# Optimization experiments

Hardware: AMD Instinct MI355X
Metric: run time of the kernel (lower is better)

## Reference

```python
import jax, jax.numpy as jnp
import numpy as np

N = 100000      # nodes
E = 1600000     # edges (avg degree 16)
D_IN, HID, D_OUT = 128, 64, 64


def setup_inputs() -> dict:
    key = jax.random.key(0)
    ks = jax.random.split(key, 32)
    rn = lambda k, shape, s=0.1: jax.random.normal(k, shape, jnp.float32) * s
    inp = {
        "x": jax.random.normal(ks[0], (N, D_IN), jnp.float32),
        "edge_index": jax.random.randint(ks[1], (2, E), 0, N, dtype=jnp.int32),
        # GAT layer 1: in=128, heads=2, C=64, concat -> 128
        "w1": rn(ks[2], (D_IN, 2 * HID)), "as1": rn(ks[3], (2, HID)),
        "ad1": rn(ks[4], (2, HID)), "b1": rn(ks[5], (2 * HID,)),
        # GAT layer 2: in=128, heads=2, C=64, concat -> 128
        "w2": rn(ks[6], (2 * HID, 2 * HID)), "as2": rn(ks[7], (2, HID)),
        "ad2": rn(ks[8], (2, HID)), "b2": rn(ks[9], (2 * HID,)),
        # GAT layer 3: in=128, heads=1, C=64, mean -> 64
        "w3": rn(ks[10], (2 * HID, D_OUT)), "as3": rn(ks[11], (1, D_OUT)),
        "ad3": rn(ks[12], (1, D_OUT)), "b3": rn(ks[13], (D_OUT,)),
        # BatchNorm (eval mode: running stats)
        "g1": 1.0 + rn(ks[14], (2 * HID,)), "be1": rn(ks[15], (2 * HID,)),
        "m1": rn(ks[16], (2 * HID,), 0.01), "v1": 1.0 + 0.1 * jax.random.uniform(ks[17], (2 * HID,)),
        "g2": 1.0 + rn(ks[18], (2 * HID,)), "be2": rn(ks[19], (2 * HID,)),
        "m2": rn(ks[20], (2 * HID,), 0.01), "v2": 1.0 + 0.1 * jax.random.uniform(ks[21], (2 * HID,)),
        "g3": 1.0 + rn(ks[22], (D_OUT,)), "be3": rn(ks[23], (D_OUT,)),
        "m3": rn(ks[24], (D_OUT,), 0.01), "v3": 1.0 + 0.1 * jax.random.uniform(ks[25], (D_OUT,)),
    }
    return inp


def _gat(h, W, a_s, a_d, b, src, dst, n, heads, concat):
    """PyG GATConv (eval, add_self_loops already applied to src/dst)."""
    C = a_s.shape[1]
    xl = (h @ W).reshape(n, heads, C)                      # [N,H,C]
    es = jnp.sum(xl * a_s, axis=-1)                        # [N,H] att_src . x
    ed = jnp.sum(xl * a_d, axis=-1)                        # [N,H]
    e = jax.nn.leaky_relu(es[src] + ed[dst], 0.2)          # [E',H]
    mx = jax.ops.segment_max(e, dst, num_segments=n)       # segment softmax over dst
    ex = jnp.exp(e - mx[dst])
    den = jax.ops.segment_sum(ex, dst, num_segments=n)
    alpha = ex / (den[dst] + 1e-16)                        # [E',H]
    out = jax.ops.segment_sum(xl[src] * alpha[:, :, None], dst, num_segments=n)
    out = out.reshape(n, heads * C) if concat else out.mean(axis=1)
    return out + b


def _bn(z, g, be, m, v):
    return (z - m) * jax.lax.rsqrt(v + 1e-5) * g + be


def reference(x, edge_index, w1, as1, ad1, b1, w2, as2, ad2, b2, w3, as3, ad3, b3,
              g1, be1, m1, v1, g2, be2, m2, v2, g3, be3, m3, v3):
    n = x.shape[0]
    loop = jnp.arange(n, dtype=edge_index.dtype)
    src = jnp.concatenate([edge_index[0], loop])           # GATConv add_self_loops=True
    dst = jnp.concatenate([edge_index[1], loop])
    z = jax.nn.relu(_bn(_gat(x, w1, as1, ad1, b1, src, dst, n, 2, True), g1, be1, m1, v1))
    z = jax.nn.relu(_bn(_gat(z, w2, as2, ad2, b2, src, dst, n, 2, True), g2, be2, m2, v2))
    z = _bn(_gat(z, w3, as3, ad3, b3, src, dst, n, 1, False), g3, be3, m3, v3)
    return z
```

## Files before the change

kernel.cpp:

```cpp
#include <hip/hip_runtime.h>
#include <hip/hip_bf16.h>
#include <cstdint>
#include <cstddef>

#define SCAN_CHUNK 2048
#define NBLK 512
#define BSH 8

typedef short bf16x8 __attribute__((ext_vector_type(8)));
typedef float f32x4 __attribute__((ext_vector_type(4)));

__device__ __forceinline__ float leaky02(float x) { return x > 0.f ? x : 0.2f * x; }
__device__ __forceinline__ float bflo(unsigned u) { return __uint_as_float(u << 16); }
__device__ __forceinline__ float bfhi(unsigned u) { return __uint_as_float(u & 0xFFFF0000u); }
__device__ __forceinline__ unsigned short f2bf(float f) {
  __hip_bfloat16 h = __float2bfloat16(f);
  return *(unsigned short*)&h;
}
__device__ __forceinline__ unsigned pack2bf(float a, float b) {
  return (unsigned)f2bf(a) | ((unsigned)f2bf(b) << 16);
}

__global__ void scan_pass1(const int* __restrict__ cnt, int* __restrict__ bsum, int n) {
  __shared__ int red[4];
  int b = blockIdx.x, t = threadIdx.x;
  int base = b * SCAN_CHUNK;
  int s = 0;
  for (int i = t; i < SCAN_CHUNK; i += 256) {
    int idx = base + i;
    if (idx < n) s += cnt[idx];
  }
  for (int off = 32; off; off >>= 1) s += __shfl_xor(s, off);
  int lane = t & 63, wid = t >> 6;
  if (lane == 0) red[wid] = s;
  __syncthreads();
  if (t == 0) bsum[b] = red[0] + red[1] + red[2] + red[3];
}

__global__ void scan_pass2(int* __restrict__ bsum, int nb, int* __restrict__ totp) {
  if (threadIdx.x == 0) {
    int run = 0;
    for (int i = 0; i < nb; ++i) { int v = bsum[i]; bsum[i] = run; run += v; }
    *totp = run;
  }
}

__global__ void scan_pass3(const int* __restrict__ cnt, const int* __restrict__ bsum,
                           int* __restrict__ out, int n) {
  __shared__ int wsum[4];
  int b = blockIdx.x, t = threadIdx.x;
  int idx0 = b * SCAN_CHUNK + t * 8;
  int vals[8];
  int s = 0;
#pragma unroll
  for (int i = 0; i < 8; ++i) {
    int id = idx0 + i;
    int v = (id < n) ? cnt[id] : 0;
    vals[i] = s; s += v;
  }
  int lane = t & 63, wid = t >> 6;
  int incl = s;
  for (int off = 1; off < 64; off <<= 1) {
    int o = __shfl_up(incl, off);
    if (lane >= off) incl += o;
  }
  if (lane == 63) wsum[wid] = incl;
  __syncthreads();
  if (t == 0) { int r = 0; for (int i = 0; i < 4; ++i) { int v = wsum[i]; wsum[i] = r; r += v; } }
  __syncthreads();
  int texcl = incl - s + wsum[wid] + bsum[b];
#pragma unroll
  for (int i = 0; i < 8; ++i) {
    int id = idx0 + i;
    if (id < n) out[id] = texcl + vals[i];
  }
}

__global__ void bucketA(const int* __restrict__ dst, int* __restrict__ H,
                        int E, int NB, int chunk) {
  __shared__ int hist[512];
  int b = blockIdx.x, t = threadIdx.x;
  hist[t] = 0; hist[t + 256] = 0;
  __syncthreads();
  int e0 = b * chunk, e1 = min(E, e0 + chunk);
  for (int e = e0 + t; e < e1; e += 256) atomicAdd(&hist[dst[e] >> BSH], 1);
  __syncthreads();
  for (int k = t; k < NB; k += 256) H[k * NBLK + b] = hist[k];
}

__global__ void bucketB(const int* __restrict__ src, const int* __restrict__ dst,
                        const int* __restrict__ O, unsigned* __restrict__ binned,
                        int E, int NB, int chunk) {
  __shared__ int cur[512];
  int b = blockIdx.x, t = threadIdx.x;
  for (int k = t; k < NB; k += 256) cur[k] = O[k * NBLK + b];
  __syncthreads();
  int e0 = b * chunk, e1 = min(E, e0 + chunk);
  for (int e = e0 + t; e < e1; e += 256) {
    int d = dst[e];
    int k = d >> BSH;
    int pos = atomicAdd(&cur[k], 1);
    binned[pos] = (unsigned)src[e] | ((unsigned)(d & 255) << 24);
  }
}

__global__ void bucketC(const unsigned* __restrict__ binned, const int* __restrict__ O,
                        int* __restrict__ rowp, int* __restrict__ col,
                        int N, int E, int NB) {
  __shared__ int cnt2[256];
  __shared__ int cur2[256];
  __shared__ int wsum[4];
  int k = blockIdx.x, t = threadIdx.x;
  int base = O[k * NBLK];
  int end  = (k + 1 < NB) ? O[(k + 1) * NBLK] : E;
  cnt2[t] = 0;
  __syncthreads();
  for (int e = base + t; e < end; e += 256) atomicAdd(&cnt2[binned[e] >> 24], 1);
  __syncthreads();
  int v = cnt2[t];
  int incl = v;
  int lane = t & 63, wid = t >> 6;
  for (int off = 1; off < 64; off <<= 1) {
    int o = __shfl_up(incl, off);
    if (lane >= off) incl += o;
  }
  if (lane == 63) wsum[wid] = incl;
  __syncthreads();
  if (t == 0) { int r = 0; for (int i = 0; i < 4; ++i) { int x = wsum[i]; wsum[i] = r; r += x; } }
  __syncthreads();
  int excl = incl - v + wsum[wid];
  int g = (k << BSH) + t;
  if (g <= N) rowp[g] = base + excl;
  cur2[t] = excl;
  __syncthreads();
  for (int e = base + t; e < end; e += 256) {
    unsigned p = binned[e];
    int pos = atomicAdd(&cur2[p >> 24], 1);
    col[base + pos] = (int)(p & 0xFFFFFFu);
  }
}

__global__ void convert_x(const float* __restrict__ x, unsigned* __restrict__ out, int n4) {
  int i = blockIdx.x * blockDim.x + threadIdx.x;
  if (i >= n4) return;
  float4 v = ((const float4*)x)[i];
  uint2 o;
  o.x = pack2bf(v.x, v.y);
  o.y = pack2bf(v.z, v.w);
  ((uint2*)out)[i] = o;
}

__global__ void prep_w(const float* __restrict__ w1, const float* __restrict__ w2,
                       const float* __restrict__ w3,
                       unsigned short* __restrict__ t1, unsigned short* __restrict__ t2,
                       unsigned short* __restrict__ t3) {
  int b = blockIdx.x, t = threadIdx.x;
  const float* W; unsigned short* T; int NO; int e;
  if (b < 64)      { W = w1; T = t1; NO = 128; e = b * 256 + t; }
  else if (b < 128){ W = w2; T = t2; NO = 128; e = (b - 64) * 256 + t; }
  else             { W = w3; T = t3; NO = 64;  e = (b - 128) * 256 + t; }
  int c = e >> 7, k = e & 127;
  T[c * 128 + k] = f2bf(W[k * NO + c]);
}

template<int NO>
__launch_bounds__(256)
__global__ void gemm_mfma(const unsigned short* __restrict__ Xb,
                          const unsigned short* __restrict__ Wt,
                          unsigned short* __restrict__ Y, int n,
                          const float* __restrict__ as, const float* __restrict__ ad,
                          float* __restrict__ es, float* __restrict__ ed) {
  constexpr int NT = NO / 16;
  const int wid = threadIdx.x >> 6, lane = threadIdx.x & 63;
  const int wr0 = (blockIdx.x * 4 + wid) * 32;
  if (wr0 >= n) return;
  const int cl = lane & 15, kg = lane >> 4;

  int r0c = wr0 + cl;      if (r0c > n - 1) r0c = n - 1;
  int r1c = wr0 + 16 + cl; if (r1c > n - 1) r1c = n - 1;
  const unsigned short* a0p = Xb + (size_t)r0c * 128 + kg * 8;
  const unsigned short* a1p = Xb + (size_t)r1c * 128 + kg * 8;
  const unsigned short* bp  = Wt + (size_t)cl * 128 + kg * 8;

  f32x4 acc[2][NT] = {};
#pragma unroll
  for (int ks = 0; ks < 4; ++ks) {
    bf16x8 a0 = *(const bf16x8*)(a0p + ks * 32);
    bf16x8 a1 = *(const bf16x8*)(a1p + ks * 32);
#pragma unroll
    for (int t = 0; t < NT; ++t) {
      bf16x8 bb = *(const bf16x8*)(bp + t * 16 * 128 + ks * 32);
      acc[0][t] = __builtin_amdgcn_mfma_f32_16x16x32_bf16(a0, bb, acc[0][t], 0, 0, 0);
      acc[1][t] = __builtin_amdgcn_mfma_f32_16x16x32_bf16(a1, bb, acc[1][t], 0, 0, 0);
    }
  }

  float asv[NT], adv[NT];
#pragma unroll
  for (int t = 0; t < NT; ++t) { asv[t] = as[t * 16 + cl]; adv[t] = ad[t * 16 + cl]; }

#pragma unroll
  for (int s = 0; s < 2; ++s) {
#pragma unroll
    for (int rg = 0; rg < 4; ++rg) {
      int r = wr0 + s * 16 + kg * 4 + rg;
      float ps0 = 0.f, pd0 = 0.f, ps1 = 0.f, pd1 = 0.f;
#pragma unroll
      for (int t = 0; t < NT; ++t) {
        float a = acc[s][t][rg];
        if (NO == 128 && t >= 4) { ps1 = fmaf(a, asv[t], ps1); pd1 = fmaf(a, adv[t], pd1); }
        else                     { ps0 = fmaf(a, asv[t], ps0); pd0 = fmaf(a, adv[t], pd0); }
      }
#pragma unroll
      for (int o = 8; o; o >>= 1) {
        ps0 += __shfl_xor(ps0, o); pd0 += __shfl_xor(pd0, o);
        if (NO == 128) { ps1 += __shfl_xor(ps1, o); pd1 += __shfl_xor(pd1, o); }
      }
      if (r < n) {
        if (cl == 0) {
          if (NO == 128) {
            es[(size_t)r * 2] = ps0; es[(size_t)r * 2 + 1] = ps1;
            ed[(size_t)r * 2] = pd0; ed[(size_t)r * 2 + 1] = pd1;
          } else {
            es[r] = ps0; ed[r] = pd0;
          }
        }
#pragma unroll
        for (int t = 0; t < NT; ++t)
          Y[(size_t)r * NO + t * 16 + cl] = f2bf(acc[s][t][rg]);
      }
    }
  }
}

__launch_bounds__(256)
__global__ void aggregate2(const unsigned short* __restrict__ xl, const float* __restrict__ es,
                           const float* __restrict__ ed, const int* __restrict__ rowp,
                           const int* __restrict__ col, const float* __restrict__ bias,
                           const float* __restrict__ g, const float* __restrict__ be,
                           const float* __restrict__ m, const float* __restrict__ v,
                           unsigned* __restrict__ out, int n) {
  int node = (blockIdx.x * blockDim.x + threadIdx.x) >> 6;
  int lane = threadIdx.x & 63;
  if (node >= n) return;
  const uint2* xr = (const uint2*)xl;
  int beg = rowp[node], end = rowp[node + 1];
  float2 edv = *(const float2*)&ed[(size_t)node * 2];
  float2 esl = *(const float2*)&es[(size_t)node * 2];
  float ws0 = __expf(leaky02(esl.x + edv.x));
  float ws1 = __expf(leaky02(esl.y + edv.y));
  float den0 = ws0, den1 = ws1;
  const int half = lane >> 5, hl = lane & 31;

  float4 acc = {0.f, 0.f, 0.f, 0.f};
  {
    float wsl = (half == 0) ? ((hl < 16) ? ws0 : ws1) : 0.f;
    uint2 sv = xr[(size_t)node * 32 + hl];
    acc.x = wsl * bflo(sv.x); acc.y = wsl * bfhi(sv.x);
    acc.z = wsl * bflo(sv.y); acc.w = wsl * bfhi(sv.y);
  }

  for (int cb = beg; cb < end; cb += 64) {
    int idx = cb + lane;
    int s = 0; float w0 = 0.f, w1 = 0.f;
    if (idx < end) {
      s = col[idx];
      float2 e2 = *(const float2*)&es[(size_t)s * 2];
      w0 = __expf(leaky02(e2.x + edv.x));
      w1 = __expf(leaky02(e2.y + edv.y));
    }
    float t0 = w0, t1 = w1;
#pragma unroll
    for (int off = 32; off; off >>= 1) { t0 += __shfl_xor(t0, off); t1 += __shfl_xor(t1, off); }
    den0 += t0; den1 += t1;

    int cend = end - cb; if (cend > 64) cend = 64;
    int i = 0;
    for (; i + 4 <= cend; i += 4) {
      int j0 = i + half, j1 = i + 2 + half;
      int s0 = __shfl(s, j0), s1 = __shfl(s, j1);
      float a00 = __shfl(w0, j0), a01 = __shfl(w1, j0);
      float a10 = __shfl(w0, j1), a11 = __shfl(w1, j1);
      uint2 v0 = xr[(size_t)s0 * 32 + hl];
      uint2 v1 = xr[(size_t)s1 * 32 + hl];
      float W0 = (hl < 16) ? a00 : a01;
      float W1 = (hl < 16) ? a10 : a11;
      acc.x = fmaf(W0, bflo(v0.x), acc.x); acc.y = fmaf(W0, bfhi(v0.x), acc.y);
      acc.z = fmaf(W0, bflo(v0.y), acc.z); acc.w = fmaf(W0, bfhi(v0.y), acc.w);
      acc.x = fmaf(W1, bflo(v1.x), acc.x); acc.y = fmaf(W1, bfhi(v1.x), acc.y);
      acc.z = fmaf(W1, bflo(v1.y), acc.z); acc.w = fmaf(W1, bfhi(v1.y), acc.w);
    }
    for (; i < cend; i += 2) {
      int j = i + half;
      int s0 = __shfl(s, j);
      float a00 = __shfl(w0, j), a01 = __shfl(w1, j);
      uint2 v0 = xr[(size_t)s0 * 32 + hl];
      float W0 = (hl < 16) ? a00 : a01;
      acc.x = fmaf(W0, bflo(v0.x), acc.x); acc.y = fmaf(W0, bfhi(v0.x), acc.y);
      acc.z = fmaf(W0, bflo(v0.y), acc.z); acc.w = fmaf(W0, bfhi(v0.y), acc.w);
    }
  }

  acc.x += __shfl_xor(acc.x, 32); acc.y += __shfl_xor(acc.y, 32);
  acc.z += __shfl_xor(acc.z, 32); acc.w += __shfl_xor(acc.w, 32);

  if (half == 0) {
    int c0 = 4 * hl;
    float den = (hl < 16) ? den0 : den1;
    float inv = 1.f / (den + 1e-16f);
    float4 bi = *(const float4*)&bias[c0];
    float4 mm = *(const float4*)&m[c0];
    float4 vv = *(const float4*)&v[c0];
    float4 gg = *(const float4*)&g[c0];
    float4 bb = *(const float4*)&be[c0];
    float r0 = (acc.x * inv + bi.x - mm.x) * rsqrtf(vv.x + 1e-5f) * gg.x + bb.x;
    float r1 = (acc.y * inv + bi.y - mm.y) * rsqrtf(vv.y + 1e-5f) * gg.y + bb.y;
    float r2 = (acc.z * inv + bi.z - mm.z) * rsqrtf(vv.z + 1e-5f) * gg.z + bb.z;
    float r3 = (acc.w * inv + bi.w - mm.w) * rsqrtf(vv.w + 1e-5f) * gg.w + bb.w;
    uint2 o;
    o.x = pack2bf(fmaxf(r0, 0.f), fmaxf(r1, 0.f));
    o.y = pack2bf(fmaxf(r2, 0.f), fmaxf(r3, 0.f));
    ((uint2*)out)[(size_t)node * 32 + hl] = o;
  }
}

__launch_bounds__(256)
__global__ void aggregate1(const unsigned short* __restrict__ xl, const float* __restrict__ es,
                           const float* __restrict__ ed, const int* __restrict__ rowp,
                           const int* __restrict__ col, const float* __restrict__ bias,
                           const float* __restrict__ g, const float* __restrict__ be,
                           const float* __restrict__ m, const float* __restrict__ v,
                           float* __restrict__ out, int n) {
  int node = (blockIdx.x * blockDim.x + threadIdx.x) >> 6;
  int lane = threadIdx.x & 63;
  if (node >= n) return;
  const uint2* xr = (const uint2*)xl;
  int beg = rowp[node], end = rowp[node + 1];
  float edv = ed[node];
  float ws = __expf(leaky02(es[node] + edv));
  float den = ws;
  const int qr = lane >> 4, hl = lane & 15;

  float4 acc = {0.f, 0.f, 0.f, 0.f};
  {
    float wsl = (qr == 0) ? ws : 0.f;
    uint2 sv = xr[(size_t)node * 16 + hl];
    acc.x = wsl * bflo(sv.x); acc.y = wsl * bfhi(sv.x);
    acc.z = wsl * bflo(sv.y); acc.w = wsl * bfhi(sv.y);
  }

  for (int cb = beg; cb < end; cb += 64) {
    int idx = cb + lane;
    int s = 0; float w = 0.f;
    if (idx < end) {
      s = col[idx];
      w = __expf(leaky02(es[s] + edv));
    }
    float t0 = w;
#pragma unroll
    for (int off = 32; off; off >>= 1) t0 += __shfl_xor(t0, off);
    den += t0;

    int cend = end - cb; if (cend > 64) cend = 64;
    int i = 0;
    for (; i + 8 <= cend; i += 8) {
      int j0 = i + qr, j1 = i + 4 + qr;
      int s0 = __shfl(s, j0), s1 = __shfl(s, j1);
      float W0 = __shfl(w, j0), W1 = __shfl(w, j1);
      uint2 v0 = xr[(size_t)s0 * 16 + hl];
      uint2 v1 = xr[(size_t)s1 * 16 + hl];
      acc.x = fmaf(W0, bflo(v0.x), acc.x); acc.y = fmaf(W0, bfhi(v0.x), acc.y);
      acc.z = fmaf(W0, bflo(v0.y), acc.z); acc.w = fmaf(W0, bfhi(v0.y), acc.w);
      acc.x = fmaf(W1, bflo(v1.x), acc.x); acc.y = fmaf(W1, bfhi(v1.x), acc.y);
      acc.z = fmaf(W1, bflo(v1.y), acc.z); acc.w = fmaf(W1, bfhi(v1.y), acc.w);
    }
    for (; i < cend; i += 4) {
      int j = i + qr;
      int s0 = __shfl(s, j);
      float W0 = __shfl(w, j);
      uint2 v0 = xr[(size_t)s0 * 16 + hl];
      acc.x = fmaf(W0, bflo(v0.x), acc.x); acc.y = fmaf(W0, bfhi(v0.x), acc.y);
      acc.z = fmaf(W0, bflo(v0.y), acc.z); acc.w = fmaf(W0, bfhi(v0.y), acc.w);
    }
  }

  acc.x += __shfl_xor(acc.x, 16); acc.y += __shfl_xor(acc.y, 16);
  acc.z += __shfl_xor(acc.z, 16); acc.w += __shfl_xor(acc.w, 16);
  acc.x += __shfl_xor(acc.x, 32); acc.y += __shfl_xor(acc.y, 32);
  acc.z += __shfl_xor(acc.z, 32); acc.w += __shfl_xor(acc.w, 32);

  if (lane < 16) {
    int c0 = 4 * hl;
    float inv = 1.f / (den + 1e-16f);
    float4 bi = *(const float4*)&bias[c0];
    float4 mm = *(const float4*)&m[c0];
    float4 vv = *(const float4*)&v[c0];
    float4 gg = *(const float4*)&g[c0];
    float4 bb = *(const float4*)&be[c0];
    float4 r;
    r.x = (acc.x * inv + bi.x - mm.x) * rsqrtf(vv.x + 1e-5f) * gg.x + bb.x;
    r.y = (acc.y * inv + bi.y - mm.y) * rsqrtf(vv.y + 1e-5f) * gg.y + bb.y;
    r.z = (acc.z * inv + bi.z - mm.z) * rsqrtf(vv.z + 1e-5f) * gg.z + bb.z;
    r.w = (acc.w * inv + bi.w - mm.w) * rsqrtf(vv.w + 1e-5f) * gg.w + bb.w;
    ((float4*)out)[(size_t)node * 16 + hl] = r;
  }
}

extern "C" void kernel_launch(void* const* d_in, const int* in_sizes, int n_in,
                              void* d_out, int out_size, void* d_ws, size_t ws_size,
                              hipStream_t stream) {
  const float* x   = (const float*)d_in[0];
  const int*   ei  = (const int*)d_in[1];
  const float* w1  = (const float*)d_in[2];
  const float* as1 = (const float*)d_in[3];
  const float* ad1 = (const float*)d_in[4];
  const float* b1  = (const float*)d_in[5];
  const float* w2  = (const float*)d_in[6];
  const float* as2 = (const float*)d_in[7];
  const float* ad2 = (const float*)d_in[8];
  const float* b2  = (const float*)d_in[9];
  const float* w3  = (const float*)d_in[10];
  const float* as3 = (const float*)d_in[11];
  const float* ad3 = (const float*)d_in[12];
  const float* b3  = (const float*)d_in[13];
  const float* g1  = (const float*)d_in[14];
  const float* be1 = (const float*)d_in[15];
  const float* m1  = (const float*)d_in[16];
  const float* v1  = (const float*)d_in[17];
  const float* g2  = (const float*)d_in[18];
  const float* be2 = (const float*)d_in[19];
  const float* m2  = (const float*)d_in[20];
  const float* v2  = (const float*)d_in[21];
  const float* g3  = (const float*)d_in[22];
  const float* be3 = (const float*)d_in[23];
  const float* m3  = (const float*)d_in[24];
  const float* v3  = (const float*)d_in[25];

  const int N = in_sizes[0] / 128;
  const int E = in_sizes[1] / 2;
  const int* srcp = ei;
  const int* dstp = ei + E;
  const int NB = (N + 255) >> BSH;
  const int M  = NB * NBLK;
  const int chunk = (E + NBLK - 1) / NBLK;

  size_t off = 0;
  auto carve = [&](size_t bytes) {
    void* p = (char*)d_ws + off;
    off += (bytes + 255) & ~(size_t)255;
    return p;
  };
  unsigned short* Xb  = (unsigned short*)carve((size_t)N * 128 * 2);
  unsigned short* Yb  = (unsigned short*)carve((size_t)N * 128 * 2);
  float* esb  = (float*)carve((size_t)N * 2 * 4);
  float* edb  = (float*)carve((size_t)N * 2 * 4);
  int*   rowp = (int*)carve((size_t)(N + 1) * 4);
  int*   col  = (int*)carve((size_t)E * 4);
  int*   H    = (int*)carve((size_t)M * 4);
  int*   O    = (int*)carve((size_t)M * 4);
  unsigned* binned = (unsigned*)carve((size_t)E * 4);
  int*   bsum = (int*)carve(256 * 4);
  int*   tot  = (int*)carve(4);
  unsigned short* Wt1 = (unsigned short*)carve(128 * 128 * 2);
  unsigned short* Wt2 = (unsigned short*)carve(128 * 128 * 2);
  unsigned short* Wt3 = (unsigned short*)carve(128 * 64 * 2);
  (void)ws_size; (void)n_in; (void)out_size;

  const int nb2 = (M + SCAN_CHUNK - 1) / SCAN_CHUNK;

  bucketA<<<NBLK, 256, 0, stream>>>(dstp, H, E, NB, chunk);
  scan_pass1<<<nb2, 256, 0, stream>>>(H, bsum, M);
  scan_pass2<<<1, 64, 0, stream>>>(bsum, nb2, tot);
  scan_pass3<<<nb2, 256, 0, stream>>>(H, bsum, O, M);
  bucketB<<<NBLK, 256, 0, stream>>>(srcp, dstp, O, binned, E, NB, chunk);
  bucketC<<<NB, 256, 0, stream>>>(binned, O, rowp, col, N, E, NB);
  convert_x<<<(N * 32 + 255) / 256, 256, 0, stream>>>(x, (unsigned*)Xb, N * 32);
  prep_w<<<160, 256, 0, stream>>>(w1, w2, w3, Wt1, Wt2, Wt3);

  const int gemm_grid = (N + 127) / 128;
  const int agg_grid = (N + 3) / 4;

  gemm_mfma<128><<<gemm_grid, 256, 0, stream>>>(Xb, Wt1, Yb, N, as1, ad1, esb, edb);
  aggregate2<<<agg_grid, 256, 0, stream>>>(Yb, esb, edb, rowp, col, b1, g1, be1, m1, v1,
                                           (unsigned*)Xb, N);
  gemm_mfma<128><<<gemm_grid, 256, 0, stream>>>(Xb, Wt2, Yb, N, as2, ad2, esb, edb);
  aggregate2<<<agg_grid, 256, 0, stream>>>(Yb, esb, edb, rowp, col, b2, g2, be2, m2, v2,
                                           (unsigned*)Xb, N);
  gemm_mfma<64><<<gemm_grid, 256, 0, stream>>>(Xb, Wt3, Yb, N, as3, ad3, esb, edb);
  aggregate1<<<agg_grid, 256, 0, stream>>>(Yb, esb, edb, rowp, col, b3, g3, be3, m3, v3,
                                           (float*)d_out, N);
}
```

Baseline: 351.1 us.

## Fold self-loops into CSR, fuse x conversion into GEMM, widen aggregation loads

Self-loop edges are now inserted into the CSR during bucketing, so the aggregation kernels no longer need a separate self-term path. The per-chunk denominator wave reduction is deferred to one final reduction. The first GEMM reads fp32 x directly and converts to bf16 in registers, which removes the convert_x kernel and its intermediate buffer. Aggregation now gathers 16-byte rows (uint4) with more edges in flight per wave, at the cost of more registers and an extra shuffle-reduction stage.

```diff
diff --git a/kernel.cpp b/kernel.cpp
--- a/kernel.cpp
+++ b/kernel.cpp
@@ -77,42 +77,50 @@
 }
 
 __global__ void bucketA(const int* __restrict__ dst, int* __restrict__ H,
-                        int E, int NB, int chunk) {
+                        int E, int N, int NB, int echunk, int nchunk) {
   __shared__ int hist[512];
   int b = blockIdx.x, t = threadIdx.x;
   hist[t] = 0; hist[t + 256] = 0;
   __syncthreads();
-  int e0 = b * chunk, e1 = min(E, e0 + chunk);
+  int e0 = b * echunk, e1 = min(E, e0 + echunk);
   for (int e = e0 + t; e < e1; e += 256) atomicAdd(&hist[dst[e] >> BSH], 1);
+  int n0 = b * nchunk, n1 = min(N, n0 + nchunk);
+  for (int nn = n0 + t; nn < n1; nn += 256) atomicAdd(&hist[nn >> BSH], 1);
   __syncthreads();
   for (int k = t; k < NB; k += 256) H[k * NBLK + b] = hist[k];
 }
 
 __global__ void bucketB(const int* __restrict__ src, const int* __restrict__ dst,
                         const int* __restrict__ O, unsigned* __restrict__ binned,
-                        int E, int NB, int chunk) {
+                        int E, int N, int NB, int echunk, int nchunk) {
   __shared__ int cur[512];
   int b = blockIdx.x, t = threadIdx.x;
   for (int k = t; k < NB; k += 256) cur[k] = O[k * NBLK + b];
   __syncthreads();
-  int e0 = b * chunk, e1 = min(E, e0 + chunk);
+  int e0 = b * echunk, e1 = min(E, e0 + echunk);
   for (int e = e0 + t; e < e1; e += 256) {
     int d = dst[e];
     int k = d >> BSH;
     int pos = atomicAdd(&cur[k], 1);
     binned[pos] = (unsigned)src[e] | ((unsigned)(d & 255) << 24);
   }
+  int n0 = b * nchunk, n1 = min(N, n0 + nchunk);
+  for (int nn = n0 + t; nn < n1; nn += 256) {
+    int k = nn >> BSH;
+    int pos = atomicAdd(&cur[k], 1);
+    binned[pos] = (unsigned)nn | ((unsigned)(nn & 255) << 24);
+  }
 }
 
 __global__ void bucketC(const unsigned* __restrict__ binned, const int* __restrict__ O,
                         int* __restrict__ rowp, int* __restrict__ col,
-                        int N, int E, int NB) {
+                        int N, int Etot, int NB) {
   __shared__ int cnt2[256];
   __shared__ int cur2[256];
   __shared__ int wsum[4];
   int k = blockIdx.x, t = threadIdx.x;
   int base = O[k * NBLK];
-  int end  = (k + 1 < NB) ? O[(k + 1) * NBLK] : E;
+  int end  = (k + 1 < NB) ? O[(k + 1) * NBLK] : Etot;
   cnt2[t] = 0;
   __syncthreads();
   for (int e = base + t; e < end; e += 256) atomicAdd(&cnt2[binned[e] >> 24], 1);
@@ -126,7 +134,7 @@
   }
   if (lane == 63) wsum[wid] = incl;
   __syncthreads();
-  if (t == 0) { int r = 0; for (int i = 0; i < 4; ++i) { int x = wsum[i]; wsum[i] = r; r += x; } }
+  if (t == 0) { int r = 0; for (int i = 0; i < 4; ++i) { int x2 = wsum[i]; wsum[i] = r; r += x2; } }
   __syncthreads();
   int excl = incl - v + wsum[wid];
   int g = (k << BSH) + t;
@@ -138,16 +146,6 @@
     int pos = atomicAdd(&cur2[p >> 24], 1);
     col[base + pos] = (int)(p & 0xFFFFFFu);
   }
-}
-
-__global__ void convert_x(const float* __restrict__ x, unsigned* __restrict__ out, int n4) {
-  int i = blockIdx.x * blockDim.x + threadIdx.x;
-  if (i >= n4) return;
-  float4 v = ((const float4*)x)[i];
-  uint2 o;
-  o.x = pack2bf(v.x, v.y);
-  o.y = pack2bf(v.z, v.w);
-  ((uint2*)out)[i] = o;
 }
 
 __global__ void prep_w(const float* __restrict__ w1, const float* __restrict__ w2,
@@ -163,9 +161,9 @@
   T[c * 128 + k] = f2bf(W[k * NO + c]);
 }
 
-template<int NO>
+template<int NO, bool F32IN>
 __launch_bounds__(256)
-__global__ void gemm_mfma(const unsigned short* __restrict__ Xb,
+__global__ void gemm_mfma(const void* __restrict__ Xp,
                           const unsigned short* __restrict__ Wt,
                           unsigned short* __restrict__ Y, int n,
                           const float* __restrict__ as, const float* __restrict__ ad,
@@ -178,18 +176,30 @@
 
   int r0c = wr0 + cl;      if (r0c > n - 1) r0c = n - 1;
   int r1c = wr0 + 16 + cl; if (r1c > n - 1) r1c = n - 1;
-  const unsigned short* a0p = Xb + (size_t)r0c * 128 + kg * 8;
-  const unsigned short* a1p = Xb + (size_t)r1c * 128 + kg * 8;
-  const unsigned short* bp  = Wt + (size_t)cl * 128 + kg * 8;
 
   f32x4 acc[2][NT] = {};
+  const unsigned short* Xb = (const unsigned short*)Xp;
+  const float* Xf = (const float*)Xp;
+
 #pragma unroll
   for (int ks = 0; ks < 4; ++ks) {
-    bf16x8 a0 = *(const bf16x8*)(a0p + ks * 32);
-    bf16x8 a1 = *(const bf16x8*)(a1p + ks * 32);
+    bf16x8 a0, a1;
+    if constexpr (F32IN) {
+      const float* p0 = Xf + (size_t)r0c * 128 + kg * 8 + ks * 32;
+      const float* p1 = Xf + (size_t)r1c * 128 + kg * 8 + ks * 32;
+      float4 u0 = *(const float4*)p0, u1 = *(const float4*)(p0 + 4);
+      float4 w0 = *(const float4*)p1, w1 = *(const float4*)(p1 + 4);
+      a0[0] = (short)f2bf(u0.x); a0[1] = (short)f2bf(u0.y); a0[2] = (short)f2bf(u0.z); a0[3] = (short)f2bf(u0.w);
+      a0[4] = (short)f2bf(u1.x); a0[5] = (short)f2bf(u1.y); a0[6] = (short)f2bf(u1.z); a0[7] = (short)f2bf(u1.w);
+      a1[0] = (short)f2bf(w0.x); a1[1] = (short)f2bf(w0.y); a1[2] = (short)f2bf(w0.z); a1[3] = (short)f2bf(w0.w);
+      a1[4] = (short)f2bf(w1.x); a1[5] = (short)f2bf(w1.y); a1[6] = (short)f2bf(w1.z); a1[7] = (short)f2bf(w1.w);
+    } else {
+      a0 = *(const bf16x8*)(Xb + (size_t)r0c * 128 + kg * 8 + ks * 32);
+      a1 = *(const bf16x8*)(Xb + (size_t)r1c * 128 + kg * 8 + ks * 32);
+    }
 #pragma unroll
     for (int t = 0; t < NT; ++t) {
-      bf16x8 bb = *(const bf16x8*)(bp + t * 16 * 128 + ks * 32);
+      bf16x8 bb = *(const bf16x8*)(Wt + (size_t)(cl + t * 16) * 128 + kg * 8 + ks * 32);
       acc[0][t] = __builtin_amdgcn_mfma_f32_16x16x32_bf16(a0, bb, acc[0][t], 0, 0, 0);
       acc[1][t] = __builtin_amdgcn_mfma_f32_16x16x32_bf16(a1, bb, acc[1][t], 0, 0, 0);
     }
@@ -239,26 +249,17 @@
                            const int* __restrict__ col, const float* __restrict__ bias,
                            const float* __restrict__ g, const float* __restrict__ be,
                            const float* __restrict__ m, const float* __restrict__ v,
-                           unsigned* __restrict__ out, int n) {
+                           uint4* __restrict__ out, int n) {
   int node = (blockIdx.x * blockDim.x + threadIdx.x) >> 6;
   int lane = threadIdx.x & 63;
   if (node >= n) return;
-  const uint2* xr = (const uint2*)xl;
+  const uint4* xr = (const uint4*)xl;
   int beg = rowp[node], end = rowp[node + 1];
   float2 edv = *(const float2*)&ed[(size_t)node * 2];
-  float2 esl = *(const float2*)&es[(size_t)node * 2];
-  float ws0 = __expf(leaky02(esl.x + edv.x));
-  float ws1 = __expf(leaky02(esl.y + edv.y));
-  float den0 = ws0, den1 = ws1;
-  const int half = lane >> 5, hl = lane & 31;
-
-  float4 acc = {0.f, 0.f, 0.f, 0.f};
-  {
-    float wsl = (half == 0) ? ((hl < 16) ? ws0 : ws1) : 0.f;
-    uint2 sv = xr[(size_t)node * 32 + hl];
-    acc.x = wsl * bflo(sv.x); acc.y = wsl * bfhi(sv.x);
-    acc.z = wsl * bflo(sv.y); acc.w = wsl * bfhi(sv.y);
-  }
+  const int q = lane >> 4, hl = lane & 15;
+
+  float acc[8] = {0.f, 0.f, 0.f, 0.f, 0.f, 0.f, 0.f, 0.f};
+  float dl0 = 0.f, dl1 = 0.f;
 
   for (int cb = beg; cb < end; cb += 64) {
     int idx = cb + lane;
@@ -269,58 +270,71 @@
       w0 = __expf(leaky02(e2.x + edv.x));
       w1 = __expf(leaky02(e2.y + edv.y));
     }
-    float t0 = w0, t1 = w1;
-#pragma unroll
-    for (int off = 32; off; off >>= 1) { t0 += __shfl_xor(t0, off); t1 += __shfl_xor(t1, off); }
-    den0 += t0; den1 += t1;
-
+    dl0 += w0; dl1 += w1;
     int cend = end - cb; if (cend > 64) cend = 64;
     int i = 0;
-    for (; i + 4 <= cend; i += 4) {
-      int j0 = i + half, j1 = i + 2 + half;
+    for (; i + 8 <= cend; i += 8) {
+      int j0 = i + q, j1 = i + 4 + q;
       int s0 = __shfl(s, j0), s1 = __shfl(s, j1);
-      float a00 = __shfl(w0, j0), a01 = __shfl(w1, j0);
-      float a10 = __shfl(w0, j1), a11 = __shfl(w1, j1);
-      uint2 v0 = xr[(size_t)s0 * 32 + hl];
-      uint2 v1 = xr[(size_t)s1 * 32 + hl];
-      float W0 = (hl < 16) ? a00 : a01;
-      float W1 = (hl < 16) ? a10 : a11;
-      acc.x = fmaf(W0, bflo(v0.x), acc.x); acc.y = fmaf(W0, bfhi(v0.x), acc.y);
-      acc.z = fmaf(W0, bflo(v0.y), acc.z); acc.w = fmaf(W0, bfhi(v0.y), acc.w);
-      acc.x = fmaf(W1, bflo(v1.x), acc.x); acc.y = fmaf(W1, bfhi(v1.x), acc.y);
-      acc.z = fmaf(W1, bflo(v1.y), acc.z); acc.w = fmaf(W1, bfhi(v1.y), acc.w);
-    }
-    for (; i < cend; i += 2) {
-      int j = i + half;
+      uint4 v0 = xr[(size_t)s0 * 16 + hl];
+      uint4 v1 = xr[(size_t)s1 * 16 + hl];
+      float w00 = __shfl(w0, j0), w01 = __shfl(w1, j0);
+      float w10 = __shfl(w0, j1), w11 = __shfl(w1, j1);
+      float W0 = (hl < 8) ? w00 : w01;
+      float W1 = (hl < 8) ? w10 : w11;
+      acc[0] = fmaf(W0, bflo(v0.x), acc[0]); acc[1] = fmaf(W0, bfhi(v0.x), acc[1]);
+      acc[2] = fmaf(W0, bflo(v0.y), acc[2]); acc[3] = fmaf(W0, bfhi(v0.y), acc[3]);
+      acc[4] = fmaf(W0, bflo(v0.z), acc[4]); acc[5] = fmaf(W0, bfhi(v0.z), acc[5]);
+      acc[6] = fmaf(W0, bflo(v0.w), acc[6]); acc[7] = fmaf(W0, bfhi(v0.w), acc[7]);
+      acc[0] = fmaf(W1, bflo(v1.x), acc[0]); acc[1] = fmaf(W1, bfhi(v1.x), acc[1]);
+      acc[2] = fmaf(W1, bflo(v1.y), acc[2]); acc[3] = fmaf(W1, bfhi(v1.y), acc[3]);
+      acc[4] = fmaf(W1, bflo(v1.z), acc[4]); acc[5] = fmaf(W1, bfhi(v1.z), acc[5]);
+      acc[6] = fmaf(W1, bflo(v1.w), acc[6]); acc[7] = fmaf(W1, bfhi(v1.w), acc[7]);
+    }
+    for (; i < cend; i += 4) {
+      int j = i + q;
       int s0 = __shfl(s, j);
-      float a00 = __shfl(w0, j), a01 = __shfl(w1, j);
-      uint2 v0 = xr[(size_t)s0 * 32 + hl];
-      float W0 = (hl < 16) ? a00 : a01;
-      acc.x = fmaf(W0, bflo(v0.x), acc.x); acc.y = fmaf(W0, bfhi(v0.x), acc.y);
-      acc.z = fmaf(W0, bflo(v0.y), acc.z); acc.w = fmaf(W0, bfhi(v0.y), acc.w);
-    }
-  }
-
-  acc.x += __shfl_xor(acc.x, 32); acc.y += __shfl_xor(acc.y, 32);
-  acc.z += __shfl_xor(acc.z, 32); acc.w += __shfl_xor(acc.w, 32);
-
-  if (half == 0) {
-    int c0 = 4 * hl;
-    float den = (hl < 16) ? den0 : den1;
+      uint4 v0 = xr[(size_t)s0 * 16 + hl];
+      float w00 = __shfl(w0, j), w01 = __shfl(w1, j);
+      float W0 = (hl < 8) ? w00 : w01;
+      acc[0] = fmaf(W0, bflo(v0.x), acc[0]); acc[1] = fmaf(W0, bfhi(v0.x), acc[1]);
+      acc[2] = fmaf(W0, bflo(v0.y), acc[2]); acc[3] = fmaf(W0, bfhi(v0.y), acc[3]);
+      acc[4] = fmaf(W0, bflo(v0.z), acc[4]); acc[5] = fmaf(W0, bfhi(v0.z), acc[5]);
+      acc[6] = fmaf(W0, bflo(v0.w), acc[6]); acc[7] = fmaf(W0, bfhi(v0.w), acc[7]);
+    }
+  }
+
+#pragma unroll
+  for (int k2 = 0; k2 < 8; ++k2) {
+    acc[k2] += __shfl_xor(acc[k2], 16);
+    acc[k2] += __shfl_xor(acc[k2], 32);
+  }
+#pragma unroll
+  for (int o = 32; o; o >>= 1) { dl0 += __shfl_xor(dl0, o); dl1 += __shfl_xor(dl1, o); }
+
+  if (q == 0) {
+    int c0 = hl * 8;
+    float den = (hl < 8) ? dl0 : dl1;
     float inv = 1.f / (den + 1e-16f);
-    float4 bi = *(const float4*)&bias[c0];
-    float4 mm = *(const float4*)&m[c0];
-    float4 vv = *(const float4*)&v[c0];
-    float4 gg = *(const float4*)&g[c0];
-    float4 bb = *(const float4*)&be[c0];
-    float r0 = (acc.x * inv + bi.x - mm.x) * rsqrtf(vv.x + 1e-5f) * gg.x + bb.x;
-    float r1 = (acc.y * inv + bi.y - mm.y) * rsqrtf(vv.y + 1e-5f) * gg.y + bb.y;
-    float r2 = (acc.z * inv + bi.z - mm.z) * rsqrtf(vv.z + 1e-5f) * gg.z + bb.z;
-    float r3 = (acc.w * inv + bi.w - mm.w) * rsqrtf(vv.w + 1e-5f) * gg.w + bb.w;
-    uint2 o;
+    float4 bi0 = *(const float4*)&bias[c0], bi1 = *(const float4*)&bias[c0 + 4];
+    float4 mm0 = *(const float4*)&m[c0],    mm1 = *(const float4*)&m[c0 + 4];
+    float4 vv0 = *(const float4*)&v[c0],    vv1 = *(const float4*)&v[c0 + 4];
+    float4 gg0 = *(const float4*)&g[c0],    gg1 = *(const float4*)&g[c0 + 4];
+    float4 bb0 = *(const float4*)&be[c0],   bb1 = *(const float4*)&be[c0 + 4];
+    float r0 = (acc[0] * inv + bi0.x - mm0.x) * rsqrtf(vv0.x + 1e-5f) * gg0.x + bb0.x;
+    float r1 = (acc[1] * inv + bi0.y - mm0.y) * rsqrtf(vv0.y + 1e-5f) * gg0.y + bb0.y;
+    float r2 = (acc[2] * inv + bi0.z - mm0.z) * rsqrtf(vv0.z + 1e-5f) * gg0.z + bb0.z;
+    float r3 = (acc[3] * inv + bi0.w - mm0.w) * rsqrtf(vv0.w + 1e-5f) * gg0.w + bb0.w;
+    float r4 = (acc[4] * inv + bi1.x - mm1.x) * rsqrtf(vv1.x + 1e-5f) * gg1.x + bb1.x;
+    float r5 = (acc[5] * inv + bi1.y - mm1.y) * rsqrtf(vv1.y + 1e-5f) * gg1.y + bb1.y;
+    float r6 = (acc[6] * inv + bi1.z - mm1.z) * rsqrtf(vv1.z + 1e-5f) * gg1.z + bb1.z;
+    float r7 = (acc[7] * inv + bi1.w - mm1.w) * rsqrtf(vv1.w + 1e-5f) * gg1.w + bb1.w;
+    uint4 o;
     o.x = pack2bf(fmaxf(r0, 0.f), fmaxf(r1, 0.f));
     o.y = pack2bf(fmaxf(r2, 0.f), fmaxf(r3, 0.f));
-    ((uint2*)out)[(size_t)node * 32 + hl] = o;
+    o.z = pack2bf(fmaxf(r4, 0.f), fmaxf(r5, 0.f));
+    o.w = pack2bf(fmaxf(r6, 0.f), fmaxf(r7, 0.f));
+    out[(size_t)node * 16 + hl] = o;
   }
 }
 
@@ -334,20 +348,13 @@
   int node = (blockIdx.x * blockDim.x + threadIdx.x) >> 6;
   int lane = threadIdx.x & 63;
   if (node >= n) return;
-  const uint2* xr = (const uint2*)xl;
+  const uint4* xr = (const uint4*)xl;
   int beg = rowp[node], end = rowp[node + 1];
   float edv = ed[node];
-  float ws = __expf(leaky02(es[node] + edv));
-  float den = ws;
-  const int qr = lane >> 4, hl = lane & 15;
-
-  float4 acc = {0.f, 0.f, 0.f, 0.f};
-  {
-    float wsl = (qr == 0) ? ws : 0.f;
-    uint2 sv = xr[(size_t)node * 16 + hl];
-    acc.x = wsl * bflo(sv.x); acc.y = wsl * bfhi(sv.x);
-    acc.z = wsl * bflo(sv.y); acc.w = wsl * bfhi(sv.y);
-  }
+  const int g8 = lane >> 3, hl = lane & 7;
+
+  float acc[8] = {0.f, 0.f, 0.f, 0.f, 0.f, 0.f, 0.f, 0.f};
+  float dl = 0.f;
 
   for (int cb = beg; cb < end; cb += 64) {
     int idx = cb + lane;
@@ -356,53 +363,64 @@
       s = col[idx];
       w = __expf(leaky02(es[s] + edv));
     }
-    float t0 = w;
-#pragma unroll
-    for (int off = 32; off; off >>= 1) t0 += __shfl_xor(t0, off);
-    den += t0;
-
+    dl += w;
     int cend = end - cb; if (cend > 64) cend = 64;
     int i = 0;
-    for (; i + 8 <= cend; i += 8) {
-      int j0 = i + qr, j1 = i + 4 + qr;
+    for (; i + 16 <= cend; i += 16) {
+      int j0 = i + g8, j1 = i + 8 + g8;
       int s0 = __shfl(s, j0), s1 = __shfl(s, j1);
+      uint4 v0 = xr[(size_t)s0 * 8 + hl];
+      uint4 v1 = xr[(size_t)s1 * 8 + hl];
       float W0 = __shfl(w, j0), W1 = __shfl(w, j1);
-      uint2 v0 = xr[(size_t)s0 * 16 + hl];
-      uint2 v1 = xr[(size_t)s1 * 16 + hl];
-      acc.x = fmaf(W0, bflo(v0.x), acc.x); acc.y = fmaf(W0, bfhi(v0.x), acc.y);
-      acc.z = fmaf(W0, bflo(v0.y), acc.z); acc.w = fmaf(W0, bfhi(v0.y), acc.w);
-      acc.x = fmaf(W1, bflo(v1.x), acc.x); acc.y = fmaf(W1, bfhi(v1.x), acc.y);
-      acc.z = fmaf(W1, bflo(v1.y), acc.z); acc.w = fmaf(W1, bfhi(v1.y), acc.w);
-    }
-    for (; i < cend; i += 4) {
-      int j = i + qr;
+      acc[0] = fmaf(W0, bflo(v0.x), acc[0]); acc[1] = fmaf(W0, bfhi(v0.x), acc[1]);
+      acc[2] = fmaf(W0, bflo(v0.y), acc[2]); acc[3] = fmaf(W0, bfhi(v0.y), acc[3]);
+      acc[4] = fmaf(W0, bflo(v0.z), acc[4]); acc[5] = fmaf(W0, bfhi(v0.z), acc[5]);
+      acc[6] = fmaf(W0, bflo(v0.w), acc[6]); acc[7] = fmaf(W0, bfhi(v0.w), acc[7]);
+      acc[0] = fmaf(W1, bflo(v1.x), acc[0]); acc[1] = fmaf(W1, bfhi(v1.x), acc[1]);
+      acc[2] = fmaf(W1, bflo(v1.y), acc[2]); acc[3] = fmaf(W1, bfhi(v1.y), acc[3]);
+      acc[4] = fmaf(W1, bflo(v1.z), acc[4]); acc[5] = fmaf(W1, bfhi(v1.z), acc[5]);
+      acc[6] = fmaf(W1, bflo(v1.w), acc[6]); acc[7] = fmaf(W1, bfhi(v1.w), acc[7]);
+    }
+    for (; i < cend; i += 8) {
+      int j = i + g8;
       int s0 = __shfl(s, j);
+      uint4 v0 = xr[(size_t)s0 * 8 + hl];
       float W0 = __shfl(w, j);
-      uint2 v0 = xr[(size_t)s0 * 16 + hl];
-      acc.x = fmaf(W0, bflo(v0.x), acc.x); acc.y = fmaf(W0, bfhi(v0.x), acc.y);
-      acc.z = fmaf(W0, bflo(v0.y), acc.z); acc.w = fmaf(W0, bfhi(v0.y), acc.w);
-    }
-  }
-
-  acc.x += __shfl_xor(acc.x, 16); acc.y += __shfl_xor(acc.y, 16);
-  acc.z += __shfl_xor(acc.z, 16); acc.w += __shfl_xor(acc.w, 16);
-  acc.x += __shfl_xor(acc.x, 32); acc.y += __shfl_xor(acc.y, 32);
-  acc.z += __shfl_xor(acc.z, 32); acc.w += __shfl_xor(acc.w, 32);
-
-  if (lane < 16) {
-    int c0 = 4 * hl;
-    float inv = 1.f / (den + 1e-16f);
-    float4 bi = *(const float4*)&bias[c0];
-    float4 mm = *(const float4*)&m[c0];
-    float4 vv = *(const float4*)&v[c0];
-    float4 gg = *(const float4*)&g[c0];
-    float4 bb = *(const float4*)&be[c0];
-    float4 r;
-    r.x = (acc.x * inv + bi.x - mm.x) * rsqrtf(vv.x + 1e-5f) * gg.x + bb.x;
-    r.y = (acc.y * inv + bi.y - mm.y) * rsqrtf(vv.y + 1e-5f) * gg.y + bb.y;
-    r.z = (acc.z * inv + bi.z - mm.z) * rsqrtf(vv.z + 1e-5f) * gg.z + bb.z;
-    r.w = (acc.w * inv + bi.w - mm.w) * rsqrtf(vv.w + 1e-5f) * gg.w + bb.w;
-    ((float4*)out)[(size_t)node * 16 + hl] = r;
+      acc[0] = fmaf(W0, bflo(v0.x), acc[0]); acc[1] = fmaf(W0, bfhi(v0.x), acc[1]);
+      acc[2] = fmaf(W0, bflo(v0.y), acc[2]); acc[3] = fmaf(W0, bfhi(v0.y), acc[3]);
+      acc[4] = fmaf(W0, bflo(v0.z), acc[4]); acc[5] = fmaf(W0, bfhi(v0.z), acc[5]);
+      acc[6] = fmaf(W0, bflo(v0.w), acc[6]); acc[7] = fmaf(W0, bfhi(v0.w), acc[7]);
+    }
+  }
+
+#pragma unroll
+  for (int k2 = 0; k2 < 8; ++k2) {
+    acc[k2] += __shfl_xor(acc[k2], 8);
+    acc[k2] += __shfl_xor(acc[k2], 16);
+    acc[k2] += __shfl_xor(acc[k2], 32);
+  }
+#pragma unroll
+  for (int o = 32; o; o >>= 1) dl += __shfl_xor(dl, o);
+
+  if (lane < 8) {
+    int c0 = hl * 8;
+    float inv = 1.f / (dl + 1e-16f);
+    float4 bi0 = *(const float4*)&bias[c0], bi1 = *(const float4*)&bias[c0 + 4];
+    float4 mm0 = *(const float4*)&m[c0],    mm1 = *(const float4*)&m[c0 + 4];
+    float4 vv0 = *(const float4*)&v[c0],    vv1 = *(const float4*)&v[c0 + 4];
+    float4 gg0 = *(const float4*)&g[c0],    gg1 = *(const float4*)&g[c0 + 4];
+    float4 bb0 = *(const float4*)&be[c0],   bb1 = *(const float4*)&be[c0 + 4];
+    float4 ra, rb;
+    ra.x = (acc[0] * inv + bi0.x - mm0.x) * rsqrtf(vv0.x + 1e-5f) * gg0.x + bb0.x;
+    ra.y = (acc[1] * inv + bi0.y - mm0.y) * rsqrtf(vv0.y + 1e-5f) * gg0.y + bb0.y;
+    ra.z = (acc[2] * inv + bi0.z - mm0.z) * rsqrtf(vv0.z + 1e-5f) * gg0.z + bb0.z;
+    ra.w = (acc[3] * inv + bi0.w - mm0.w) * rsqrtf(vv0.w + 1e-5f) * gg0.w + bb0.w;
+    rb.x = (acc[4] * inv + bi1.x - mm1.x) * rsqrtf(vv1.x + 1e-5f) * gg1.x + bb1.x;
+    rb.y = (acc[5] * inv + bi1.y - mm1.y) * rsqrtf(vv1.y + 1e-5f) * gg1.y + bb1.y;
+    rb.z = (acc[6] * inv + bi1.z - mm1.z) * rsqrtf(vv1.z + 1e-5f) * gg1.z + bb1.z;
+    rb.w = (acc[7] * inv + bi1.w - mm1.w) * rsqrtf(vv1.w + 1e-5f) * gg1.w + bb1.w;
+    float4* op = (float4*)(out + (size_t)node * 64 + c0);
+    op[0] = ra; op[1] = rb;
   }
 }
 
@@ -438,11 +456,13 @@
 
   const int N = in_sizes[0] / 128;
   const int E = in_sizes[1] / 2;
+  const int Etot = E + N;
   const int* srcp = ei;
   const int* dstp = ei + E;
   const int NB = (N + 255) >> BSH;
   const int M  = NB * NBLK;
-  const int chunk = (E + NBLK - 1) / NBLK;
+  const int echunk = (E + NBLK - 1) / NBLK;
+  const int nchunk = (N + NBLK - 1) / NBLK;
 
   size_t off = 0;
   auto carve = [&](size_t bytes) {
@@ -455,10 +475,10 @@
   float* esb  = (float*)carve((size_t)N * 2 * 4);
   float* edb  = (float*)carve((size_t)N * 2 * 4);
   int*   rowp = (int*)carve((size_t)(N + 1) * 4);
-  int*   col  = (int*)carve((size_t)E * 4);
+  int*   col  = (int*)carve((size_t)Etot * 4);
   int*   H    = (int*)carve((size_t)M * 4);
   int*   O    = (int*)carve((size_t)M * 4);
-  unsigned* binned = (unsigned*)carve((size_t)E * 4);
+  unsigned* binned = (unsigned*)carve((size_t)Etot * 4);
   int*   bsum = (int*)carve(256 * 4);
   int*   tot  = (int*)carve(4);
   unsigned short* Wt1 = (unsigned short*)carve(128 * 128 * 2);
@@ -468,25 +488,24 @@
 
   const int nb2 = (M + SCAN_CHUNK - 1) / SCAN_CHUNK;
 
-  bucketA<<<NBLK, 256, 0, stream>>>(dstp, H, E, NB, chunk);
+  bucketA<<<NBLK, 256, 0, stream>>>(dstp, H, E, N, NB, echunk, nchunk);
   scan_pass1<<<nb2, 256, 0, stream>>>(H, bsum, M);
   scan_pass2<<<1, 64, 0, stream>>>(bsum, nb2, tot);
   scan_pass3<<<nb2, 256, 0, stream>>>(H, bsum, O, M);
-  bucketB<<<NBLK, 256, 0, stream>>>(srcp, dstp, O, binned, E, NB, chunk);
-  bucketC<<<NB, 256, 0, stream>>>(binned, O, rowp, col, N, E, NB);
-  convert_x<<<(N * 32 + 255) / 256, 256, 0, stream>>>(x, (unsigned*)Xb, N * 32);
+  bucketB<<<NBLK, 256, 0, stream>>>(srcp, dstp, O, binned, E, N, NB, echunk, nchunk);
+  bucketC<<<NB, 256, 0, stream>>>(binned, O, rowp, col, N, Etot, NB);
   prep_w<<<160, 256, 0, stream>>>(w1, w2, w3, Wt1, Wt2, Wt3);
 
   const int gemm_grid = (N + 127) / 128;
   const int agg_grid = (N + 3) / 4;
 
-  gemm_mfma<128><<<gemm_grid, 256, 0, stream>>>(Xb, Wt1, Yb, N, as1, ad1, esb, edb);
+  gemm_mfma<128, true><<<gemm_grid, 256, 0, stream>>>(x, Wt1, Yb, N, as1, ad1, esb, edb);
   aggregate2<<<agg_grid, 256, 0, stream>>>(Yb, esb, edb, rowp, col, b1, g1, be1, m1, v1,
-                                           (unsigned*)Xb, N);
-  gemm_mfma<128><<<gemm_grid, 256, 0, stream>>>(Xb, Wt2, Yb, N, as2, ad2, esb, edb);
+                                           (uint4*)Xb, N);
+  gemm_mfma<128, false><<<gemm_grid, 256, 0, stream>>>(Xb, Wt2, Yb, N, as2, ad2, esb, edb);
   aggregate2<<<agg_grid, 256, 0, stream>>>(Yb, esb, edb, rowp, col, b2, g2, be2, m2, v2,
-                                           (unsigned*)Xb, N);
-  gemm_mfma<64><<<gemm_grid, 256, 0, stream>>>(Xb, Wt3, Yb, N, as3, ad3, esb, edb);
+                                           (uint4*)Xb, N);
+  gemm_mfma<64, false><<<gemm_grid, 256, 0, stream>>>(Xb, Wt3, Yb, N, as3, ad3, esb, edb);
   aggregate1<<<agg_grid, 256, 0, stream>>>(Yb, esb, edb, rowp, col, b3, g3, be3, m3, v3,
                                            (float*)d_out, N);
 }
```

Result: no change. 344.5 us (-1.9%).
